# Kernel optimization log

Hardware: AMD Instinct MI355X
Metric: run time of the kernel (lower is better)

The kernel has to match this reference:

```python
import jax, jax.numpy as jnp
import numpy as np

B = 2048
IN_FEATURES = 512
OUT_FEATURES = 32768
S = 64.0   # arcface default scale
M = 0.5    # arcface default margin
EPS = 1e-7


def _l2_normalize(x, axis=-1):
    # matches torch F.normalize(p=2, eps=1e-12)
    n = jnp.sqrt(jnp.sum(x * x, axis=axis, keepdims=True))
    return x / jnp.maximum(n, 1e-12)


def setup_inputs() -> dict:
    key = jax.random.key(0)
    k1, k2, k3 = jax.random.split(key, 3)
    features = jax.random.normal(k1, (B, IN_FEATURES), dtype=jnp.float32)
    y_true = jax.random.randint(k2, (B,), 0, OUT_FEATURES)
    # xavier_uniform_ for weight of shape (out, in)
    limit = float(np.sqrt(6.0 / (OUT_FEATURES + IN_FEATURES)))
    weight = jax.random.uniform(k3, (OUT_FEATURES, IN_FEATURES), dtype=jnp.float32,
                                minval=-limit, maxval=limit)
    return {"features": features, "y_true": y_true, "weight": weight}


def reference(features, y_true, weight):
    f = _l2_normalize(features)            # [B, D]
    w = _l2_normalize(weight)              # [C, D]
    wf = jnp.einsum('bd,cd->bc', f, w)     # [B, C] cosine logits
    tgt = wf[jnp.arange(wf.shape[0]), y_true]  # [B]
    # arcface margin transform
    numerator = S * jnp.cos(jnp.arccos(jnp.clip(tgt, -1.0 + EPS, 1.0 - EPS)) + M)
    # sum of exp(s*wf) over all non-target classes = full sum minus target term
    excl_sum = jnp.sum(jnp.exp(S * wf), axis=1) - jnp.exp(S * tgt)
    denominator = jnp.exp(numerator) + excl_sum
    L = numerator - jnp.log(denominator)
    return -jnp.mean(L)
```

## Files before the change

### kernel.cpp

```cpp
#include <hip/hip_runtime.h>
#include <hip/hip_bf16.h>
#include <math.h>


#define BN 2048
#define DK 512
#define CN 32768

typedef __attribute__((ext_vector_type(4))) float floatx4;
typedef __attribute__((ext_vector_type(16))) float floatx16;
typedef __attribute__((ext_vector_type(2))) long longx2;
typedef __attribute__((ext_vector_type(4))) long longx4;
typedef __attribute__((ext_vector_type(8))) int intx8;

__device__ inline float dot4(floatx4 a, floatx4 b) {
  return a.x * b.x + a.y * b.y + a.z * b.z + a.w * b.w;
}

__device__ inline int pack_fp8x4(floatx4 v) {
  int r = __builtin_amdgcn_cvt_pk_fp8_f32(v.x, v.y, 0, false);
  r = __builtin_amdgcn_cvt_pk_fp8_f32(v.z, v.w, r, true);
  return r;
}

__device__ inline int permute16(int j) {
  return ((j >> 1) & 3) * 4 + (j >> 3) * 2 + (j & 1);
}

__device__ inline void async_ld16(const void* g, void* l) {
  __builtin_amdgcn_global_load_lds(
      (const __attribute__((address_space(1))) void*)g,
      (__attribute__((address_space(3))) void*)l, 16, 0, 0);
}

__global__ void prep_kernel(const float* __restrict__ feat,
                            const int* __restrict__ y,
                            const float* __restrict__ w,
                            int* __restrict__ fb8,
                            int* __restrict__ wb8,
                            float* __restrict__ tgt,
                            float* __restrict__ rowsum) {
  const int wave = threadIdx.x >> 6;
  const int l = threadIdx.x & 63;
  const int d0 = ((l >> 4) * 16)       + permute16(l & 15);
  const int d1 = ((4 + (l >> 4)) * 16) + permute16(l & 15);
  if (blockIdx.x < 8192) {
    const int row = blockIdx.x * 4 + wave;
    const floatx4* src = (const floatx4*)(w + (size_t)row * DK);
    floatx4 v0 = src[l];
    floatx4 v1 = src[64 + l];
    float s = dot4(v0, v0) + dot4(v1, v1);
#pragma unroll
    for (int off = 1; off < 64; off <<= 1) s += __shfl_xor(s, off, 64);
    const float scale = 1.0f / fmaxf(sqrtf(s), 1e-12f);
    v0 *= scale; v1 *= scale;
    int* db = wb8 + (size_t)row * 128;
    db[d0] = pack_fp8x4(v0);
    db[d1] = pack_fp8x4(v1);
  } else {
    const int i = (blockIdx.x - 8192) * 4 + wave;
    const floatx4* src = (const floatx4*)(feat + (size_t)i * DK);
    floatx4 v0 = src[l];
    floatx4 v1 = src[64 + l];
    const int cls = y[i];
    const floatx4* wr = (const floatx4*)(w + (size_t)cls * DK);
    floatx4 w0 = wr[l], w1 = wr[64 + l];
    float s  = dot4(v0, v0) + dot4(v1, v1);
    float d  = dot4(v0, w0) + dot4(v1, w1);
    float wn = dot4(w0, w0) + dot4(w1, w1);
#pragma unroll
    for (int off = 1; off < 64; off <<= 1) {
      s  += __shfl_xor(s, off, 64);
      d  += __shfl_xor(d, off, 64);
      wn += __shfl_xor(wn, off, 64);
    }
    const float fscale = 1.0f / fmaxf(sqrtf(s), 1e-12f);
    v0 *= fscale; v1 *= fscale;
    int* db = fb8 + (size_t)i * 128;
    db[d0] = pack_fp8x4(v0);
    db[d1] = pack_fp8x4(v1);
    if (l == 0) {
      tgt[i] = d * fscale / fmaxf(sqrtf(wn), 1e-12f);
      rowsum[i] = 0.0f;
    }
  }
}

__launch_bounds__(512, 4)
__global__ void gemm_exp_kernel(const char* __restrict__ fb8,
                                const char* __restrict__ wb8,
                                float* __restrict__ rowsum) {
  __shared__ char As[2][2 * 128 * 64];
  __shared__ char Bs[2][2 * 128 * 64];
  __shared__ float lsum[128];

  const int tid  = threadIdx.x;
  const int wave = tid >> 6;
  const int lane = tid & 63;

  const int n = blockIdx.x;
  const int tileM = ((n >> 3) & 15) * 128;
  const int tileN = (((n >> 7) << 3) | (n & 7)) * 128;

  const int wm = (wave & 3) * 32;
  const int wn = (wave >> 2) * 64;

  if (tid < 128) lsum[tid] = 0.0f;

  floatx16 acc[2];
#pragma unroll
  for (int tj = 0; tj < 2; ++tj)
#pragma unroll
    for (int r = 0; r < 16; ++r)
      acc[tj][r] = 0.0f;

  const int rowL = tid >> 2;
  const int uL   = (tid & 3) ^ ((rowL >> 1) & 3);
  const char* gA = fb8 + (size_t)(tileM + rowL) * DK + uL * 16;
  const char* gB = wb8 + (size_t)(tileN + rowL) * DK + uL * 16;
  const int ldsO = wave * 1024;

  const int r31 = lane & 31;
  const int q2  = (lane >> 5) * 2;
  int offA0, offA1, offB0[2], offB1[2];
  {
    const int row = wm + r31;
    const int rot = (row >> 1) & 3;
    offA0 = row * 64 + ((q2    ) ^ rot) * 16;
    offA1 = row * 64 + ((q2 + 1) ^ rot) * 16;
  }
#pragma unroll
  for (int tj = 0; tj < 2; ++tj) {
    const int row = wn + tj * 32 + r31;
    const int rot = (row >> 1) & 3;
    offB0[tj] = row * 64 + ((q2    ) ^ rot) * 16;
    offB1[tj] = row * 64 + ((q2 + 1) ^ rot) * 16;
  }

  async_ld16(gA,      &As[0][ldsO]);
  async_ld16(gA + 64, &As[0][8192 + ldsO]);
  async_ld16(gB,      &Bs[0][ldsO]);
  async_ld16(gB + 64, &Bs[0][8192 + ldsO]);
  gA += 128; gB += 128;

#pragma unroll
  for (int it = 0; it < DK / 128; ++it) {
    const int cur = it & 1;
    __syncthreads();
    if (it < DK / 128 - 1) {
      const int nxt = cur ^ 1;
      async_ld16(gA,      &As[nxt][ldsO]);
      async_ld16(gA + 64, &As[nxt][8192 + ldsO]);
      async_ld16(gB,      &Bs[nxt][ldsO]);
      async_ld16(gB + 64, &Bs[nxt][8192 + ldsO]);
      gA += 128; gB += 128;
    }

#pragma unroll
    for (int ks = 0; ks < 2; ++ks) {
      const char* Ab = &As[cur][ks * 8192];
      const char* Bb = &Bs[cur][ks * 8192];
      intx8 a, b[2];
      {
        longx2 lo = *(const longx2*)(Ab + offA0);
        longx2 hi = *(const longx2*)(Ab + offA1);
        a = (intx8)(longx4){lo.x, lo.y, hi.x, hi.y};
      }
#pragma unroll
      for (int tj = 0; tj < 2; ++tj) {
        longx2 lo = *(const longx2*)(Bb + offB0[tj]);
        longx2 hi = *(const longx2*)(Bb + offB1[tj]);
        b[tj] = (intx8)(longx4){lo.x, lo.y, hi.x, hi.y};
      }
#pragma unroll
      for (int tj = 0; tj < 2; ++tj)
        acc[tj] = __builtin_amdgcn_mfma_scale_f32_32x32x64_f8f6f4(
            a, b[tj], acc[tj],
            0, 0, 0, 0x7f7f7f7f, 0, 0x7f7f7f7f);
    }
  }

  const int qrow = (lane >> 5) * 4;
#pragma unroll
  for (int r = 0; r < 16; ++r) {
    float v = __expf(64.0f * acc[0][r]) + __expf(64.0f * acc[1][r]);
    v += __shfl_xor(v, 1, 64);
    v += __shfl_xor(v, 2, 64);
    v += __shfl_xor(v, 4, 64);
    v += __shfl_xor(v, 8, 64);
    v += __shfl_xor(v, 16, 64);
    if ((lane & 31) == 0)
      atomicAdd(&lsum[wm + qrow + (r & 3) + 8 * (r >> 2)], v);
  }
  __syncthreads();
  if (tid < 128)
    atomicAdd(&rowsum[tileM + tid], lsum[tid]);
}

__global__ void loss_kernel(const float* __restrict__ tgt,
                            const float* __restrict__ rowsum,
                            float* __restrict__ out) {
  __shared__ float wsum[8];
  const int t = threadIdx.x;
  float sum = 0.f;
  const float cM = 0.87758256189037271f;
  const float sM = 0.47942553860420301f;
  for (int i = t; i < BN; i += 512) {
    const float tg_raw = tgt[i];
    const float tg = fminf(fmaxf(tg_raw, -1.f + 1e-7f), 1.f - 1e-7f);
    const float num = 64.f * (tg * cM - sqrtf(fmaxf(1.f - tg * tg, 0.f)) * sM);
    const float den = expf(num) + rowsum[i] - expf(64.f * tg_raw);
    sum += num - logf(den);
  }
#pragma unroll
  for (int off = 1; off < 64; off <<= 1) sum += __shfl_xor(sum, off, 64);
  if ((t & 63) == 0) wsum[t >> 6] = sum;
  __syncthreads();
  if (t == 0) {
    float tot = 0.f;
#pragma unroll
    for (int k = 0; k < 8; ++k) tot += wsum[k];
    out[0] = -tot * (1.0f / (float)BN);
  }
}

extern "C" void kernel_launch(void* const* d_in, const int* in_sizes, int n_in,
                              void* d_out, int out_size, void* d_ws, size_t ws_size,
                              hipStream_t stream) {
  const float* features = (const float*)d_in[0];
  const int*   y_true   = (const int*)d_in[1];
  const float* weight   = (const float*)d_in[2];
  float* out = (float*)d_out;

  char* ws = (char*)d_ws;
  char* wb8    = ws;
  char* fb8    = ws + 16777216;
  float* tgt    = (float*)(ws + 17825792);
  float* rowsum = (float*)(ws + 17833984);

  prep_kernel<<<8192 + 512, 256, 0, stream>>>(features, y_true, weight,
                                              (int*)fb8, (int*)wb8, tgt, rowsum);
  gemm_exp_kernel<<<4096, 512, 0, stream>>>(fb8, wb8, rowsum);
  loss_kernel<<<1, 512, 0, stream>>>(tgt, rowsum, out);
}
```

Before: 169.7 us.

## Load A operand directly from global into registers and use DPP row reductions

The feature (A) tile is no longer staged through LDS. Each lane loads its MFMA A fragment straight from global memory into a double-buffered register prefetch array, which removes the LDS traffic and LDS reads for A. The epilogue's xor-shuffle reduction is replaced with DPP row_shr and row_bcast adds, with the final sum taken at lane 31 of each half-wave. The cost is more registers and uncoalesced 16-byte global loads for A, which may pressure occupancy under launch_bounds(512,4).

```diff
diff --git a/kernel.cpp b/kernel.cpp
--- a/kernel.cpp
+++ b/kernel.cpp
@@ -31,6 +31,13 @@
   __builtin_amdgcn_global_load_lds(
       (const __attribute__((address_space(1))) void*)g,
       (__attribute__((address_space(3))) void*)l, 16, 0, 0);
+}
+
+template <int CTRL>
+__device__ inline float dpp_add(float v) {
+  int t = __builtin_amdgcn_update_dpp(0, __float_as_int(v), CTRL, 0xf, 0xf,
+                                      true);
+  return v + __int_as_float(t);
 }
 
 __global__ void prep_kernel(const float* __restrict__ feat,
@@ -90,7 +97,6 @@
 __global__ void gemm_exp_kernel(const char* __restrict__ fb8,
                                 const char* __restrict__ wb8,
                                 float* __restrict__ rowsum) {
-  __shared__ char As[2][2 * 128 * 64];
   __shared__ char Bs[2][2 * 128 * 64];
   __shared__ float lsum[128];
 
@@ -116,19 +122,15 @@
 
   const int rowL = tid >> 2;
   const int uL   = (tid & 3) ^ ((rowL >> 1) & 3);
-  const char* gA = fb8 + (size_t)(tileM + rowL) * DK + uL * 16;
   const char* gB = wb8 + (size_t)(tileN + rowL) * DK + uL * 16;
   const int ldsO = wave * 1024;
 
   const int r31 = lane & 31;
   const int q2  = (lane >> 5) * 2;
-  int offA0, offA1, offB0[2], offB1[2];
-  {
-    const int row = wm + r31;
-    const int rot = (row >> 1) & 3;
-    offA0 = row * 64 + ((q2    ) ^ rot) * 16;
-    offA1 = row * 64 + ((q2 + 1) ^ rot) * 16;
-  }
+  const longx2* gA = (const longx2*)(fb8 + (size_t)(tileM + wm + r31) * DK
+                                     + q2 * 16);
+
+  int offB0[2], offB1[2];
 #pragma unroll
   for (int tj = 0; tj < 2; ++tj) {
     const int row = wn + tj * 32 + r31;
@@ -137,11 +139,14 @@
     offB1[tj] = row * 64 + ((q2 + 1) ^ rot) * 16;
   }
 
-  async_ld16(gA,      &As[0][ldsO]);
-  async_ld16(gA + 64, &As[0][8192 + ldsO]);
+  longx2 apre[2][2][2];
+
   async_ld16(gB,      &Bs[0][ldsO]);
   async_ld16(gB + 64, &Bs[0][8192 + ldsO]);
-  gA += 128; gB += 128;
+  gB += 128;
+  apre[0][0][0] = gA[0];  apre[0][0][1] = gA[1];
+  apre[0][1][0] = gA[4];  apre[0][1][1] = gA[5];
+  gA += 8;
 
 #pragma unroll
   for (int it = 0; it < DK / 128; ++it) {
@@ -149,23 +154,20 @@
     __syncthreads();
     if (it < DK / 128 - 1) {
       const int nxt = cur ^ 1;
-      async_ld16(gA,      &As[nxt][ldsO]);
-      async_ld16(gA + 64, &As[nxt][8192 + ldsO]);
       async_ld16(gB,      &Bs[nxt][ldsO]);
       async_ld16(gB + 64, &Bs[nxt][8192 + ldsO]);
-      gA += 128; gB += 128;
+      gB += 128;
+      apre[nxt][0][0] = gA[0];  apre[nxt][0][1] = gA[1];
+      apre[nxt][1][0] = gA[4];  apre[nxt][1][1] = gA[5];
+      gA += 8;
     }
 
 #pragma unroll
     for (int ks = 0; ks < 2; ++ks) {
-      const char* Ab = &As[cur][ks * 8192];
       const char* Bb = &Bs[cur][ks * 8192];
       intx8 a, b[2];
-      {
-        longx2 lo = *(const longx2*)(Ab + offA0);
-        longx2 hi = *(const longx2*)(Ab + offA1);
-        a = (intx8)(longx4){lo.x, lo.y, hi.x, hi.y};
-      }
+      a = (intx8)(longx4){apre[cur][ks][0].x, apre[cur][ks][0].y,
+                          apre[cur][ks][1].x, apre[cur][ks][1].y};
 #pragma unroll
       for (int tj = 0; tj < 2; ++tj) {
         longx2 lo = *(const longx2*)(Bb + offB0[tj]);
@@ -184,12 +186,12 @@
 #pragma unroll
   for (int r = 0; r < 16; ++r) {
     float v = __expf(64.0f * acc[0][r]) + __expf(64.0f * acc[1][r]);
-    v += __shfl_xor(v, 1, 64);
-    v += __shfl_xor(v, 2, 64);
-    v += __shfl_xor(v, 4, 64);
-    v += __shfl_xor(v, 8, 64);
-    v += __shfl_xor(v, 16, 64);
-    if ((lane & 31) == 0)
+    v = dpp_add<0x111>(v);
+    v = dpp_add<0x112>(v);
+    v = dpp_add<0x114>(v);
+    v = dpp_add<0x118>(v);
+    v = dpp_add<0x142>(v);
+    if ((lane & 31) == 31)
       atomicAdd(&lsum[wm + qrow + (r & 3) + 8 * (r >> 2)], v);
   }
   __syncthreads();
```

New measurement: 174.5 us. +2.9%, slower.
